# Kernel optimization log

Hardware: AMD Instinct MI355X
Metric: run time of the kernel (lower is better)

## Reference

```python
import jax, jax.numpy as jnp
import numpy as np

DIM = 128

def setup_inputs() -> dict:
    key = jax.random.key(0)
    ks = jax.random.split(key, 4)
    N, C, L = 64, DIM, 4096
    scale = 1.0 / np.sqrt(DIM)
    return {
        "x": jax.random.normal(ks[0], (N, C, L), dtype=jnp.float32),
        "Wq": jax.random.normal(ks[1], (DIM, DIM), dtype=jnp.float32) * scale,
        "bq": jnp.zeros((DIM,), dtype=jnp.float32),
        "Wk": jax.random.normal(ks[2], (DIM, DIM), dtype=jnp.float32) * scale,
        "bk": jnp.zeros((DIM,), dtype=jnp.float32),
        "Wv": jax.random.normal(ks[3], (DIM, DIM), dtype=jnp.float32) * scale,
        "bv": jnp.zeros((DIM,), dtype=jnp.float32),
    }

def reference(x, Wq, bq, Wk, bk, Wv, bv):
    # x: [N, C, L] -> rearrange to [N, L, C]
    h = jnp.transpose(x, (0, 2, 1))                       # [N, L, C]
    q = jnp.einsum('nlc,cd->nld', h, Wq) + bq             # [N, L, D]
    k = jnp.einsum('nlc,cd->nld', h, Wk) + bk             # [N, L, D]
    v = jnp.einsum('nlc,cd->nld', h, Wv) + bv             # [N, L, D]
    # AFT-Simple: softmax over sequence axis of K, global weighted pool of V
    w = jax.nn.softmax(k, axis=1)                         # [N, L, D]
    pooled = jnp.sum(w * v, axis=1, keepdims=True)        # [N, 1, D]
    out = jax.nn.sigmoid(q) * pooled                      # [N, L, D]
    return jnp.transpose(out, (0, 2, 1))                  # [N, C, L]
```

## Files before the change

### kernel.cpp

```cpp
#include <hip/hip_runtime.h>
#include <hip/hip_bf16.h>

#define NB 64
#define CD 128
#define LL 4096
#define LCHUNK 64
#define NCHUNK 64

typedef __attribute__((ext_vector_type(8))) short short8;
typedef __attribute__((ext_vector_type(4))) float f32x4;

#define LOG2E 1.4426950408889634f

#define WT_OFF   0
#define WSS_OFF  (1u<<20)
#define WSP_OFF  ((1u<<20) + NB*NCHUNK*CD*4)
#define POOL_OFF ((1u<<20) + 2u*NB*NCHUNK*CD*4)
#define WSQ_OFF  (8u<<20)

__device__ __forceinline__ unsigned short f2bf(float f) {
    union { float f; unsigned u; } v; v.f = f;
    unsigned r = v.u + 0x7FFFu + ((v.u >> 16) & 1u);
    return (unsigned short)(r >> 16);
}
__device__ __forceinline__ float bf2f(unsigned short h) {
    union { unsigned u; float f; } v; v.u = ((unsigned)h) << 16;
    return v.f;
}
__device__ __forceinline__ unsigned pack2(float lo, float hi) {
    union { __hip_bfloat162 h; unsigned u; } v;
    v.h = __float22bfloat162_rn(float2{lo, hi});
    return v.u;
}

__global__ void prep_wt(const float* __restrict__ Wq, const float* __restrict__ Wk,
                        const float* __restrict__ Wv, unsigned short* __restrict__ wt) {
    int t = blockIdx.x >> 7;
    int d = blockIdx.x & 127;
    const float* W = (t == 0) ? Wq : (t == 1) ? Wk : Wv;
    int c = threadIdx.x;
    wt[((size_t)t*CD + d)*CD + c] = f2bf(W[c*CD + d]);
}

__global__ __launch_bounds__(256, 4)
void aft_pass1(const float* __restrict__ x, const unsigned short* __restrict__ wt,
               const float* __restrict__ bq, const float* __restrict__ bk,
               const float* __restrict__ bv,
               float* __restrict__ wsS, float* __restrict__ wsP,
               unsigned short* __restrict__ wsq) {
    __shared__ char lds_x[64 * 272];
    __shared__ unsigned short lds_q[CD * 68];
    const int tid = threadIdx.x;
    const int n = blockIdx.x >> 6;
    const int ch = blockIdx.x & 63;
    const int l0 = ch * LCHUNK;
    const int w = tid >> 6, lane = tid & 63, r = lane & 15, g = lane >> 4;

    {
        const int f = tid & 15;
        const int tg = tid >> 4;
        const int sw = 16 * 272 * 0 + 0; (void)sw;
#pragma unroll
        for (int it = 0; it < 4; ++it) {
            int cp = tg + 16*it;
            int c0 = 2*cp;
            f32x4 lo = *(const f32x4*)(x + ((size_t)n*CD + c0    )*LL + l0 + 4*f);
            f32x4 hi = *(const f32x4*)(x + ((size_t)n*CD + c0 + 1)*LL + l0 + 4*f);
            int B  = cp >> 2;
            int go = cp & 3;
            char* base = lds_x + (4*f)*272 + 16*(B ^ (f & 7)) + 4*go;
#pragma unroll
            for (int j = 0; j < 4; ++j)
                *(unsigned*)(base + j*272) = pack2(lo[j], hi[j]);
        }
    }

    short8 a_k[2][4], a_v[2][4];
#pragma unroll
    for (int rt = 0; rt < 2; ++rt)
#pragma unroll
        for (int s = 0; s < 4; ++s) {
            int d = 32*w + 16*rt + r;
            a_k[rt][s] = *(const short8*)(wt + ((size_t)(1*CD + d))*CD + 32*s + 8*g);
            a_v[rt][s] = *(const short8*)(wt + ((size_t)(2*CD + d))*CD + 32*s + 8*g);
        }
    f32x4 bkv[2], bvv[2];
#pragma unroll
    for (int rt = 0; rt < 2; ++rt) {
        bkv[rt] = *(const f32x4*)(bk + 32*w + 16*rt + 4*g);
        bvv[rt] = *(const f32x4*)(bv + 32*w + 16*rt + 4*g);
    }

    __syncthreads();

    float s_run[2][4], p_run[2][4];
#pragma unroll
    for (int rt = 0; rt < 2; ++rt)
#pragma unroll
        for (int v = 0; v < 4; ++v) { s_run[rt][v] = 0.f; p_run[rt][v] = 0.f; }

#pragma unroll 1
    for (int ct = 0; ct < 4; ++ct) {
        f32x4 ak[2], av[2];
#pragma unroll
        for (int rt = 0; rt < 2; ++rt) {
            ak[rt] = (f32x4){0.f,0.f,0.f,0.f};
            av[rt] = (f32x4){0.f,0.f,0.f,0.f};
        }
        const int lrow = 16*ct + r;
        const int lsw = (lrow >> 2) & 7;
#pragma unroll
        for (int s = 0; s < 4; ++s) {
            const short8 b = *(const short8*)(lds_x + lrow*272 + 16*((4*s + g) ^ lsw));
            ak[0] = __builtin_amdgcn_mfma_f32_16x16x32_bf16(a_k[0][s], b, ak[0], 0,0,0);
            ak[1] = __builtin_amdgcn_mfma_f32_16x16x32_bf16(a_k[1][s], b, ak[1], 0,0,0);
            av[0] = __builtin_amdgcn_mfma_f32_16x16x32_bf16(a_v[0][s], b, av[0], 0,0,0);
            av[1] = __builtin_amdgcn_mfma_f32_16x16x32_bf16(a_v[1][s], b, av[1], 0,0,0);
        }
#pragma unroll
        for (int rt = 0; rt < 2; ++rt)
#pragma unroll
            for (int v = 0; v < 4; ++v) {
                float e = __builtin_amdgcn_exp2f((ak[rt][v] + bkv[rt][v]) * LOG2E);
                s_run[rt][v] += e;
                p_run[rt][v] += e * (av[rt][v] + bvv[rt][v]);
            }
    }

    short8 a_q[2][4];
#pragma unroll
    for (int rt = 0; rt < 2; ++rt)
#pragma unroll
        for (int s = 0; s < 4; ++s) {
            int d = 32*w + 16*rt + r;
            a_q[rt][s] = *(const short8*)(wt + ((size_t)(0*CD + d))*CD + 32*s + 8*g);
        }
    f32x4 bqv[2];
#pragma unroll
    for (int rt = 0; rt < 2; ++rt)
        bqv[rt] = *(const f32x4*)(bq + 32*w + 16*rt + 4*g);

#pragma unroll 1
    for (int ct = 0; ct < 4; ++ct) {
        f32x4 aq[2];
        aq[0] = (f32x4){0.f,0.f,0.f,0.f};
        aq[1] = (f32x4){0.f,0.f,0.f,0.f};
        const int lrow = 16*ct + r;
        const int lsw = (lrow >> 2) & 7;
#pragma unroll
        for (int s = 0; s < 4; ++s) {
            const short8 b = *(const short8*)(lds_x + lrow*272 + 16*((4*s + g) ^ lsw));
            aq[0] = __builtin_amdgcn_mfma_f32_16x16x32_bf16(a_q[0][s], b, aq[0], 0,0,0);
            aq[1] = __builtin_amdgcn_mfma_f32_16x16x32_bf16(a_q[1][s], b, aq[1], 0,0,0);
        }
#pragma unroll
        for (int rt = 0; rt < 2; ++rt)
#pragma unroll
            for (int v = 0; v < 4; ++v) {
                float q2 = (aq[rt][v] + bqv[rt][v]) * LOG2E;
                float sg = __builtin_amdgcn_rcpf(1.f + __builtin_amdgcn_exp2f(-q2));
                lds_q[(32*w + 16*rt + 4*g + v)*68 + ct*16 + r] = f2bf(sg);
            }
    }

#pragma unroll
    for (int rt = 0; rt < 2; ++rt)
#pragma unroll
        for (int v = 0; v < 4; ++v) {
            float s = s_run[rt][v], p = p_run[rt][v];
#pragma unroll
            for (int mask = 1; mask <= 8; mask <<= 1) {
                s += __shfl_xor(s, mask, 64);
                p += __shfl_xor(p, mask, 64);
            }
            if (r == 0) {
                int d = 32*w + 16*rt + 4*g + v;
                size_t idx = ((size_t)n*NCHUNK + ch)*CD + d;
                wsS[idx] = s;
                wsP[idx] = p;
            }
        }

    __syncthreads();
    {
        unsigned short* tile = wsq + ((size_t)(n*NCHUNK + ch)) * (CD*LCHUNK);
        const int col = tid & 7;
#pragma unroll
        for (int it = 0; it < 4; ++it) {
            int row = (tid >> 3) + 32*it;
            short8 val = *(const short8*)(lds_q + row*68 + 8*col);
            *(short8*)(tile + row*LCHUNK + 8*col) = val;
        }
    }
}

__global__ void aft_pass2(const float* __restrict__ wsS, const float* __restrict__ wsP,
                          float* __restrict__ pooled) {
    int n = blockIdx.x, d = threadIdx.x;
    float s = 0.f, p = 0.f;
    for (int b = 0; b < NCHUNK; ++b) {
        size_t idx = ((size_t)n*NCHUNK + b)*CD + d;
        s += wsS[idx];
        p += wsP[idx];
    }
    pooled[(size_t)n*CD + d] = p / s;
}

__global__ __launch_bounds__(256)
void aft_pass3(const unsigned short* __restrict__ wsq, const float* __restrict__ pooled,
               float* __restrict__ out) {
    __shared__ float lpool[CD];
    const int n = blockIdx.x >> 6;
    const int ch = blockIdx.x & 63;
    if (threadIdx.x < CD) lpool[threadIdx.x] = pooled[(size_t)n*CD + threadIdx.x];
    __syncthreads();
    const unsigned short* tile = wsq + ((size_t)(n*NCHUNK + ch)) * (CD*LCHUNK);
    const int l0 = ch * LCHUNK;
#pragma unroll
    for (int it = 0; it < 4; ++it) {
        int gi = threadIdx.x + 256*it;
        int row = gi >> 3, col = gi & 7;
        short8 v = *(const short8*)(tile + row*LCHUNK + 8*col);
        float pl = lpool[row];
        f32x4 o0, o1;
#pragma unroll
        for (int j = 0; j < 4; ++j) {
            o0[j] = bf2f((unsigned short)v[j]) * pl;
            o1[j] = bf2f((unsigned short)v[4+j]) * pl;
        }
        float* dst = out + ((size_t)n*CD + row)*LL + l0 + 8*col;
        *(f32x4*)dst = o0;
        *(f32x4*)(dst + 4) = o1;
    }
}

extern "C" void kernel_launch(void* const* d_in, const int* in_sizes, int n_in,
                              void* d_out, int out_size, void* d_ws, size_t ws_size,
                              hipStream_t stream) {
    const float* x  = (const float*)d_in[0];
    const float* Wq = (const float*)d_in[1];
    const float* bq = (const float*)d_in[2];
    const float* Wk = (const float*)d_in[3];
    const float* bk = (const float*)d_in[4];
    const float* Wv = (const float*)d_in[5];
    const float* bv = (const float*)d_in[6];
    float* out = (float*)d_out;
    char* ws = (char*)d_ws;
    unsigned short* wt = (unsigned short*)(ws + WT_OFF);
    float* wsS = (float*)(ws + WSS_OFF);
    float* wsP = (float*)(ws + WSP_OFF);
    float* pooled = (float*)(ws + POOL_OFF);
    unsigned short* wsq = (unsigned short*)(ws + WSQ_OFF);

    prep_wt<<<384, 128, 0, stream>>>(Wq, Wk, Wv, wt);
    aft_pass1<<<NB * NCHUNK, 256, 0, stream>>>(x, wt, bq, bk, bv, wsS, wsP, wsq);
    aft_pass2<<<NB, CD, 0, stream>>>(wsS, wsP, pooled);
    aft_pass3<<<NB * NCHUNK, 256, 0, stream>>>(wsq, pooled, out);
}
```

Baseline: 122.1 us.

## Make pass1 persistent over eight chunks with register-prefetched x tiles

Pass1 now launches 512 blocks of 512 threads, and each block loops over 8 consecutive L-chunks. The next chunk's x is prefetched into registers while the current one is computed, and the Q/K/V weight fragments are loaded once per block instead of once per chunk. Q, K and V MFMAs are fused into one loop, the sigmoid tile is packed to bf16 pairs through LDS, and partial sums are reduced per block group, which shrinks the pass2 reduction. The trade-off is fewer blocks (512 vs 4096) and extra barriers per iteration, so occupancy and latency hiding may suffer.

```diff
diff --git a/kernel.cpp b/kernel.cpp
--- a/kernel.cpp
+++ b/kernel.cpp
@@ -6,16 +6,19 @@
 #define LL 4096
 #define LCHUNK 64
 #define NCHUNK 64
+#define NT 8
+#define NBG 8
 
 typedef __attribute__((ext_vector_type(8))) short short8;
 typedef __attribute__((ext_vector_type(4))) float f32x4;
+typedef __attribute__((ext_vector_type(4))) unsigned u32x4;
 
 #define LOG2E 1.4426950408889634f
 
 #define WT_OFF   0
 #define WSS_OFF  (1u<<20)
-#define WSP_OFF  ((1u<<20) + NB*NCHUNK*CD*4)
-#define POOL_OFF ((1u<<20) + 2u*NB*NCHUNK*CD*4)
+#define WSP_OFF  ((1u<<20) + NB*NBG*CD*4)
+#define POOL_OFF ((1u<<20) + 2u*NB*NBG*CD*4)
 #define WSQ_OFF  (8u<<20)
 
 __device__ __forceinline__ unsigned short f2bf(float f) {
@@ -42,154 +45,122 @@
     wt[((size_t)t*CD + d)*CD + c] = f2bf(W[c*CD + d]);
 }
 
-__global__ __launch_bounds__(256, 4)
+__global__ __launch_bounds__(512, 4)
 void aft_pass1(const float* __restrict__ x, const unsigned short* __restrict__ wt,
                const float* __restrict__ bq, const float* __restrict__ bk,
                const float* __restrict__ bv,
                float* __restrict__ wsS, float* __restrict__ wsP,
                unsigned short* __restrict__ wsq) {
     __shared__ char lds_x[64 * 272];
-    __shared__ unsigned short lds_q[CD * 68];
+    __shared__ unsigned lds_t[CD * 33];
     const int tid = threadIdx.x;
-    const int n = blockIdx.x >> 6;
-    const int ch = blockIdx.x & 63;
-    const int l0 = ch * LCHUNK;
-    const int w = tid >> 6, lane = tid & 63, r = lane & 15, g = lane >> 4;
+    const int n = blockIdx.x >> 3;
+    const int bg = blockIdx.x & 7;
+    const int ww = tid >> 6, lane = tid & 63, r = lane & 15, g = lane >> 4;
+    const int f = tid & 15, tg = tid >> 4;
+
+    short8 a_q[4], a_k[4], a_v[4];
+#pragma unroll
+    for (int s = 0; s < 4; ++s) {
+        int d = 16*ww + r;
+        a_q[s] = *(const short8*)(wt + ((size_t)(0*CD + d))*CD + 32*s + 8*g);
+        a_k[s] = *(const short8*)(wt + ((size_t)(1*CD + d))*CD + 32*s + 8*g);
+        a_v[s] = *(const short8*)(wt + ((size_t)(2*CD + d))*CD + 32*s + 8*g);
+    }
+    const f32x4 bqv = *(const f32x4*)(bq + 16*ww + 4*g);
+    const f32x4 bkv = *(const f32x4*)(bk + 16*ww + 4*g);
+    const f32x4 bvv = *(const f32x4*)(bv + 16*ww + 4*g);
+
+    float s_run[4] = {0.f,0.f,0.f,0.f}, p_run[4] = {0.f,0.f,0.f,0.f};
+
+    f32x4 rx0, rx1, rx2, rx3;
+    const size_t xbase = (size_t)n*CD*LL;
 
     {
-        const int f = tid & 15;
-        const int tg = tid >> 4;
-        const int sw = 16 * 272 * 0 + 0; (void)sw;
-#pragma unroll
-        for (int it = 0; it < 4; ++it) {
-            int cp = tg + 16*it;
-            int c0 = 2*cp;
-            f32x4 lo = *(const f32x4*)(x + ((size_t)n*CD + c0    )*LL + l0 + 4*f);
-            f32x4 hi = *(const f32x4*)(x + ((size_t)n*CD + c0 + 1)*LL + l0 + 4*f);
-            int B  = cp >> 2;
-            int go = cp & 3;
-            char* base = lds_x + (4*f)*272 + 16*(B ^ (f & 7)) + 4*go;
-#pragma unroll
-            for (int j = 0; j < 4; ++j)
-                *(unsigned*)(base + j*272) = pack2(lo[j], hi[j]);
-        }
-    }
-
-    short8 a_k[2][4], a_v[2][4];
-#pragma unroll
-    for (int rt = 0; rt < 2; ++rt)
-#pragma unroll
-        for (int s = 0; s < 4; ++s) {
-            int d = 32*w + 16*rt + r;
-            a_k[rt][s] = *(const short8*)(wt + ((size_t)(1*CD + d))*CD + 32*s + 8*g);
-            a_v[rt][s] = *(const short8*)(wt + ((size_t)(2*CD + d))*CD + 32*s + 8*g);
-        }
-    f32x4 bkv[2], bvv[2];
-#pragma unroll
-    for (int rt = 0; rt < 2; ++rt) {
-        bkv[rt] = *(const f32x4*)(bk + 32*w + 16*rt + 4*g);
-        bvv[rt] = *(const f32x4*)(bv + 32*w + 16*rt + 4*g);
-    }
-
-    __syncthreads();
-
-    float s_run[2][4], p_run[2][4];
-#pragma unroll
-    for (int rt = 0; rt < 2; ++rt)
-#pragma unroll
-        for (int v = 0; v < 4; ++v) { s_run[rt][v] = 0.f; p_run[rt][v] = 0.f; }
-
-#pragma unroll 1
-    for (int ct = 0; ct < 4; ++ct) {
-        f32x4 ak[2], av[2];
-#pragma unroll
-        for (int rt = 0; rt < 2; ++rt) {
-            ak[rt] = (f32x4){0.f,0.f,0.f,0.f};
-            av[rt] = (f32x4){0.f,0.f,0.f,0.f};
-        }
-        const int lrow = 16*ct + r;
-        const int lsw = (lrow >> 2) & 7;
-#pragma unroll
-        for (int s = 0; s < 4; ++s) {
-            const short8 b = *(const short8*)(lds_x + lrow*272 + 16*((4*s + g) ^ lsw));
-            ak[0] = __builtin_amdgcn_mfma_f32_16x16x32_bf16(a_k[0][s], b, ak[0], 0,0,0);
-            ak[1] = __builtin_amdgcn_mfma_f32_16x16x32_bf16(a_k[1][s], b, ak[1], 0,0,0);
-            av[0] = __builtin_amdgcn_mfma_f32_16x16x32_bf16(a_v[0][s], b, av[0], 0,0,0);
-            av[1] = __builtin_amdgcn_mfma_f32_16x16x32_bf16(a_v[1][s], b, av[1], 0,0,0);
-        }
-#pragma unroll
-        for (int rt = 0; rt < 2; ++rt)
+        const int l0 = (bg*NT) * LCHUNK;
+        rx0 = *(const f32x4*)(x + xbase + (size_t)(2*tg    )*LL + l0 + 4*f);
+        rx1 = *(const f32x4*)(x + xbase + (size_t)(2*tg + 1)*LL + l0 + 4*f);
+        rx2 = *(const f32x4*)(x + xbase + (size_t)(2*(tg+32)    )*LL + l0 + 4*f);
+        rx3 = *(const f32x4*)(x + xbase + (size_t)(2*(tg+32) + 1)*LL + l0 + 4*f);
+    }
+
+    for (int t = 0; t < NT; ++t) {
+        const int ch = bg*NT + t;
+        __syncthreads();
+        {
+            char* base0 = lds_x + (4*f)*272 + 16*((tg>>2) ^ (f & 7)) + 4*(tg & 3);
+            char* base1 = lds_x + (4*f)*272 + 16*(((tg+32)>>2) ^ (f & 7)) + 4*((tg+32) & 3);
+#pragma unroll
+            for (int j = 0; j < 4; ++j) {
+                *(unsigned*)(base0 + j*272) = pack2(rx0[j], rx1[j]);
+                *(unsigned*)(base1 + j*272) = pack2(rx2[j], rx3[j]);
+            }
+        }
+        __syncthreads();
+        if (t + 1 < NT) {
+            const int l0 = (ch + 1) * LCHUNK;
+            rx0 = *(const f32x4*)(x + xbase + (size_t)(2*tg    )*LL + l0 + 4*f);
+            rx1 = *(const f32x4*)(x + xbase + (size_t)(2*tg + 1)*LL + l0 + 4*f);
+            rx2 = *(const f32x4*)(x + xbase + (size_t)(2*(tg+32)    )*LL + l0 + 4*f);
+            rx3 = *(const f32x4*)(x + xbase + (size_t)(2*(tg+32) + 1)*LL + l0 + 4*f);
+        }
+#pragma unroll
+        for (int ct = 0; ct < 4; ++ct) {
+            f32x4 aq = (f32x4){0.f,0.f,0.f,0.f};
+            f32x4 ak = (f32x4){0.f,0.f,0.f,0.f};
+            f32x4 av = (f32x4){0.f,0.f,0.f,0.f};
+            const int lrow = 16*ct + r;
+            const int lsw = (lrow >> 2) & 7;
+#pragma unroll
+            for (int s = 0; s < 4; ++s) {
+                const short8 b = *(const short8*)(lds_x + lrow*272 + 16*((4*s + g) ^ lsw));
+                aq = __builtin_amdgcn_mfma_f32_16x16x32_bf16(a_q[s], b, aq, 0,0,0);
+                ak = __builtin_amdgcn_mfma_f32_16x16x32_bf16(a_k[s], b, ak, 0,0,0);
+                av = __builtin_amdgcn_mfma_f32_16x16x32_bf16(a_v[s], b, av, 0,0,0);
+            }
+            float sg[4];
 #pragma unroll
             for (int v = 0; v < 4; ++v) {
-                float e = __builtin_amdgcn_exp2f((ak[rt][v] + bkv[rt][v]) * LOG2E);
-                s_run[rt][v] += e;
-                p_run[rt][v] += e * (av[rt][v] + bvv[rt][v]);
-            }
-    }
-
-    short8 a_q[2][4];
-#pragma unroll
-    for (int rt = 0; rt < 2; ++rt)
-#pragma unroll
-        for (int s = 0; s < 4; ++s) {
-            int d = 32*w + 16*rt + r;
-            a_q[rt][s] = *(const short8*)(wt + ((size_t)(0*CD + d))*CD + 32*s + 8*g);
-        }
-    f32x4 bqv[2];
-#pragma unroll
-    for (int rt = 0; rt < 2; ++rt)
-        bqv[rt] = *(const f32x4*)(bq + 32*w + 16*rt + 4*g);
-
-#pragma unroll 1
-    for (int ct = 0; ct < 4; ++ct) {
-        f32x4 aq[2];
-        aq[0] = (f32x4){0.f,0.f,0.f,0.f};
-        aq[1] = (f32x4){0.f,0.f,0.f,0.f};
-        const int lrow = 16*ct + r;
-        const int lsw = (lrow >> 2) & 7;
-#pragma unroll
-        for (int s = 0; s < 4; ++s) {
-            const short8 b = *(const short8*)(lds_x + lrow*272 + 16*((4*s + g) ^ lsw));
-            aq[0] = __builtin_amdgcn_mfma_f32_16x16x32_bf16(a_q[0][s], b, aq[0], 0,0,0);
-            aq[1] = __builtin_amdgcn_mfma_f32_16x16x32_bf16(a_q[1][s], b, aq[1], 0,0,0);
-        }
-#pragma unroll
-        for (int rt = 0; rt < 2; ++rt)
+                float e = __builtin_amdgcn_exp2f((ak[v] + bkv[v]) * LOG2E);
+                s_run[v] += e;
+                p_run[v] += e * (av[v] + bvv[v]);
+                float q2 = (aq[v] + bqv[v]) * LOG2E;
+                sg[v] = __builtin_amdgcn_rcpf(1.f + __builtin_amdgcn_exp2f(-q2));
+            }
 #pragma unroll
             for (int v = 0; v < 4; ++v) {
-                float q2 = (aq[rt][v] + bqv[rt][v]) * LOG2E;
-                float sg = __builtin_amdgcn_rcpf(1.f + __builtin_amdgcn_exp2f(-q2));
-                lds_q[(32*w + 16*rt + 4*g + v)*68 + ct*16 + r] = f2bf(sg);
-            }
-    }
-
-#pragma unroll
-    for (int rt = 0; rt < 2; ++rt)
-#pragma unroll
-        for (int v = 0; v < 4; ++v) {
-            float s = s_run[rt][v], p = p_run[rt][v];
-#pragma unroll
-            for (int mask = 1; mask <= 8; mask <<= 1) {
-                s += __shfl_xor(s, mask, 64);
-                p += __shfl_xor(p, mask, 64);
-            }
-            if (r == 0) {
-                int d = 32*w + 16*rt + 4*g + v;
-                size_t idx = ((size_t)n*NCHUNK + ch)*CD + d;
-                wsS[idx] = s;
-                wsP[idx] = p;
-            }
-        }
-
-    __syncthreads();
-    {
-        unsigned short* tile = wsq + ((size_t)(n*NCHUNK + ch)) * (CD*LCHUNK);
-        const int col = tid & 7;
-#pragma unroll
-        for (int it = 0; it < 4; ++it) {
-            int row = (tid >> 3) + 32*it;
-            short8 val = *(const short8*)(lds_q + row*68 + 8*col);
-            *(short8*)(tile + row*LCHUNK + 8*col) = val;
+                float other = __shfl_xor(sg[v], 1, 64);
+                if (!(lane & 1))
+                    lds_t[(16*ww + 4*g + v)*33 + 8*ct + (r >> 1)] = pack2(sg[v], other);
+            }
+        }
+        __syncthreads();
+        {
+            unsigned short* tile = wsq + ((size_t)(n*NCHUNK + ch)) * (CD*LCHUNK);
+            const int row = tid >> 2, part = tid & 3;
+            const unsigned* src = lds_t + row*33 + part*8;
+            u32x4 A, B;
+#pragma unroll
+            for (int k = 0; k < 4; ++k) { A[k] = src[k]; B[k] = src[4+k]; }
+            unsigned short* dst = tile + row*LCHUNK + part*16;
+            *(u32x4*)dst = A;
+            *(u32x4*)(dst + 8) = B;
+        }
+    }
+
+#pragma unroll
+    for (int v = 0; v < 4; ++v) {
+        float s = s_run[v], p = p_run[v];
+#pragma unroll
+        for (int mask = 1; mask <= 8; mask <<= 1) {
+            s += __shfl_xor(s, mask, 64);
+            p += __shfl_xor(p, mask, 64);
+        }
+        if (r == 0) {
+            int d = 16*ww + 4*g + v;
+            size_t idx = ((size_t)n*NBG + bg)*CD + d;
+            wsS[idx] = s;
+            wsP[idx] = p;
         }
     }
 }
@@ -198,8 +169,8 @@
                           float* __restrict__ pooled) {
     int n = blockIdx.x, d = threadIdx.x;
     float s = 0.f, p = 0.f;
-    for (int b = 0; b < NCHUNK; ++b) {
-        size_t idx = ((size_t)n*NCHUNK + b)*CD + d;
+    for (int b = 0; b < NBG; ++b) {
+        size_t idx = ((size_t)n*NBG + b)*CD + d;
         s += wsS[idx];
         p += wsP[idx];
     }
@@ -253,7 +224,7 @@
     unsigned short* wsq = (unsigned short*)(ws + WSQ_OFF);
 
     prep_wt<<<384, 128, 0, stream>>>(Wq, Wk, Wv, wt);
-    aft_pass1<<<NB * NCHUNK, 256, 0, stream>>>(x, wt, bq, bk, bv, wsS, wsP, wsq);
+    aft_pass1<<<NB * NBG, 512, 0, stream>>>(x, wt, bq, bk, bv, wsS, wsP, wsq);
     aft_pass2<<<NB, CD, 0, stream>>>(wsS, wsP, pooled);
     aft_pass3<<<NB * NCHUNK, 256, 0, stream>>>(wsq, pooled, out);
 }
```

New measurement: 162.0 us. 1.33x slower.

## Recompute q from x in output pass instead of storing bf16 q workspace

Applied to the files above, without the earlier changes.

Splits the first pass into a K/V-only reduction kernel and moves the Q projection plus sigmoid into the final output kernel, which re-stages x and writes the output directly. This removes the bf16 q write and read through global workspace but re-reads x a second time. MFMA operands are swapped so each lane owns a feature column, simplifying the cross-lane reduction and bias loads.

```diff
diff --git a/kernel.cpp b/kernel.cpp
--- a/kernel.cpp
+++ b/kernel.cpp
@@ -16,16 +16,11 @@
 #define WSS_OFF  (1u<<20)
 #define WSP_OFF  ((1u<<20) + NB*NCHUNK*CD*4)
 #define POOL_OFF ((1u<<20) + 2u*NB*NCHUNK*CD*4)
-#define WSQ_OFF  (8u<<20)
 
 __device__ __forceinline__ unsigned short f2bf(float f) {
     union { float f; unsigned u; } v; v.f = f;
     unsigned r = v.u + 0x7FFFu + ((v.u >> 16) & 1u);
     return (unsigned short)(r >> 16);
-}
-__device__ __forceinline__ float bf2f(unsigned short h) {
-    union { unsigned u; float f; } v; v.u = ((unsigned)h) << 16;
-    return v.f;
 }
 __device__ __forceinline__ unsigned pack2(float lo, float hi) {
     union { __hip_bfloat162 h; unsigned u; } v;
@@ -42,154 +37,88 @@
     wt[((size_t)t*CD + d)*CD + c] = f2bf(W[c*CD + d]);
 }
 
+__device__ __forceinline__ void stage_x(const float* __restrict__ x, char* lds_x,
+                                        int n, int l0, int tid) {
+    const int f = tid & 15, tg = tid >> 4;
+#pragma unroll
+    for (int it = 0; it < 4; ++it) {
+        int cp = tg + 16*it;
+        f32x4 lo = *(const f32x4*)(x + ((size_t)n*CD + 2*cp    )*LL + l0 + 4*f);
+        f32x4 hi = *(const f32x4*)(x + ((size_t)n*CD + 2*cp + 1)*LL + l0 + 4*f);
+        char* base = lds_x + (4*f)*272 + 16*((cp >> 2) ^ (f & 7)) + 4*(cp & 3);
+#pragma unroll
+        for (int j = 0; j < 4; ++j)
+            *(unsigned*)(base + j*272) = pack2(lo[j], hi[j]);
+    }
+}
+
 __global__ __launch_bounds__(256, 4)
-void aft_pass1(const float* __restrict__ x, const unsigned short* __restrict__ wt,
-               const float* __restrict__ bq, const float* __restrict__ bk,
-               const float* __restrict__ bv,
-               float* __restrict__ wsS, float* __restrict__ wsP,
-               unsigned short* __restrict__ wsq) {
+void aft_kv(const float* __restrict__ x, const unsigned short* __restrict__ wt,
+            const float* __restrict__ bk, const float* __restrict__ bv,
+            float* __restrict__ wsS, float* __restrict__ wsP) {
     __shared__ char lds_x[64 * 272];
-    __shared__ unsigned short lds_q[CD * 68];
     const int tid = threadIdx.x;
     const int n = blockIdx.x >> 6;
     const int ch = blockIdx.x & 63;
     const int l0 = ch * LCHUNK;
     const int w = tid >> 6, lane = tid & 63, r = lane & 15, g = lane >> 4;
 
-    {
-        const int f = tid & 15;
-        const int tg = tid >> 4;
-        const int sw = 16 * 272 * 0 + 0; (void)sw;
-#pragma unroll
-        for (int it = 0; it < 4; ++it) {
-            int cp = tg + 16*it;
-            int c0 = 2*cp;
-            f32x4 lo = *(const f32x4*)(x + ((size_t)n*CD + c0    )*LL + l0 + 4*f);
-            f32x4 hi = *(const f32x4*)(x + ((size_t)n*CD + c0 + 1)*LL + l0 + 4*f);
-            int B  = cp >> 2;
-            int go = cp & 3;
-            char* base = lds_x + (4*f)*272 + 16*(B ^ (f & 7)) + 4*go;
-#pragma unroll
-            for (int j = 0; j < 4; ++j)
-                *(unsigned*)(base + j*272) = pack2(lo[j], hi[j]);
-        }
-    }
-
-    short8 a_k[2][4], a_v[2][4];
-#pragma unroll
-    for (int rt = 0; rt < 2; ++rt)
+    short8 b_k[2][4], b_v[2][4];
+    float bkl[2], bvl[2];
+#pragma unroll
+    for (int dt = 0; dt < 2; ++dt) {
+        int d = 32*w + 16*dt + r;
 #pragma unroll
         for (int s = 0; s < 4; ++s) {
-            int d = 32*w + 16*rt + r;
-            a_k[rt][s] = *(const short8*)(wt + ((size_t)(1*CD + d))*CD + 32*s + 8*g);
-            a_v[rt][s] = *(const short8*)(wt + ((size_t)(2*CD + d))*CD + 32*s + 8*g);
-        }
-    f32x4 bkv[2], bvv[2];
-#pragma unroll
-    for (int rt = 0; rt < 2; ++rt) {
-        bkv[rt] = *(const f32x4*)(bk + 32*w + 16*rt + 4*g);
-        bvv[rt] = *(const f32x4*)(bv + 32*w + 16*rt + 4*g);
-    }
-
+            b_k[dt][s] = *(const short8*)(wt + ((size_t)(1*CD + d))*CD + 32*s + 8*g);
+            b_v[dt][s] = *(const short8*)(wt + ((size_t)(2*CD + d))*CD + 32*s + 8*g);
+        }
+        bkl[dt] = bk[d];
+        bvl[dt] = bv[d];
+    }
+
+    stage_x(x, lds_x, n, l0, tid);
     __syncthreads();
 
-    float s_run[2][4], p_run[2][4];
-#pragma unroll
-    for (int rt = 0; rt < 2; ++rt)
-#pragma unroll
-        for (int v = 0; v < 4; ++v) { s_run[rt][v] = 0.f; p_run[rt][v] = 0.f; }
-
-#pragma unroll 1
-    for (int ct = 0; ct < 4; ++ct) {
+    float s_run[2] = {0.f, 0.f}, p_run[2] = {0.f, 0.f};
+
+#pragma unroll
+    for (int lt = 0; lt < 4; ++lt) {
+        const int lrow = 16*lt + r;
+        const int lsw = (lrow >> 2) & 7;
+        short8 a[4];
+#pragma unroll
+        for (int s = 0; s < 4; ++s)
+            a[s] = *(const short8*)(lds_x + lrow*272 + 16*((4*s + g) ^ lsw));
         f32x4 ak[2], av[2];
 #pragma unroll
-        for (int rt = 0; rt < 2; ++rt) {
-            ak[rt] = (f32x4){0.f,0.f,0.f,0.f};
-            av[rt] = (f32x4){0.f,0.f,0.f,0.f};
-        }
-        const int lrow = 16*ct + r;
-        const int lsw = (lrow >> 2) & 7;
+        for (int dt = 0; dt < 2; ++dt) { ak[dt] = (f32x4){0,0,0,0}; av[dt] = (f32x4){0,0,0,0}; }
 #pragma unroll
         for (int s = 0; s < 4; ++s) {
-            const short8 b = *(const short8*)(lds_x + lrow*272 + 16*((4*s + g) ^ lsw));
-            ak[0] = __builtin_amdgcn_mfma_f32_16x16x32_bf16(a_k[0][s], b, ak[0], 0,0,0);
-            ak[1] = __builtin_amdgcn_mfma_f32_16x16x32_bf16(a_k[1][s], b, ak[1], 0,0,0);
-            av[0] = __builtin_amdgcn_mfma_f32_16x16x32_bf16(a_v[0][s], b, av[0], 0,0,0);
-            av[1] = __builtin_amdgcn_mfma_f32_16x16x32_bf16(a_v[1][s], b, av[1], 0,0,0);
-        }
-#pragma unroll
-        for (int rt = 0; rt < 2; ++rt)
+            ak[0] = __builtin_amdgcn_mfma_f32_16x16x32_bf16(a[s], b_k[0][s], ak[0], 0,0,0);
+            ak[1] = __builtin_amdgcn_mfma_f32_16x16x32_bf16(a[s], b_k[1][s], ak[1], 0,0,0);
+            av[0] = __builtin_amdgcn_mfma_f32_16x16x32_bf16(a[s], b_v[0][s], av[0], 0,0,0);
+            av[1] = __builtin_amdgcn_mfma_f32_16x16x32_bf16(a[s], b_v[1][s], av[1], 0,0,0);
+        }
+#pragma unroll
+        for (int dt = 0; dt < 2; ++dt)
 #pragma unroll
             for (int v = 0; v < 4; ++v) {
-                float e = __builtin_amdgcn_exp2f((ak[rt][v] + bkv[rt][v]) * LOG2E);
-                s_run[rt][v] += e;
-                p_run[rt][v] += e * (av[rt][v] + bvv[rt][v]);
+                float e = __builtin_amdgcn_exp2f((ak[dt][v] + bkl[dt]) * LOG2E);
+                s_run[dt] += e;
+                p_run[dt] += e * (av[dt][v] + bvl[dt]);
             }
     }
 
-    short8 a_q[2][4];
-#pragma unroll
-    for (int rt = 0; rt < 2; ++rt)
-#pragma unroll
-        for (int s = 0; s < 4; ++s) {
-            int d = 32*w + 16*rt + r;
-            a_q[rt][s] = *(const short8*)(wt + ((size_t)(0*CD + d))*CD + 32*s + 8*g);
-        }
-    f32x4 bqv[2];
-#pragma unroll
-    for (int rt = 0; rt < 2; ++rt)
-        bqv[rt] = *(const f32x4*)(bq + 32*w + 16*rt + 4*g);
-
-#pragma unroll 1
-    for (int ct = 0; ct < 4; ++ct) {
-        f32x4 aq[2];
-        aq[0] = (f32x4){0.f,0.f,0.f,0.f};
-        aq[1] = (f32x4){0.f,0.f,0.f,0.f};
-        const int lrow = 16*ct + r;
-        const int lsw = (lrow >> 2) & 7;
-#pragma unroll
-        for (int s = 0; s < 4; ++s) {
-            const short8 b = *(const short8*)(lds_x + lrow*272 + 16*((4*s + g) ^ lsw));
-            aq[0] = __builtin_amdgcn_mfma_f32_16x16x32_bf16(a_q[0][s], b, aq[0], 0,0,0);
-            aq[1] = __builtin_amdgcn_mfma_f32_16x16x32_bf16(a_q[1][s], b, aq[1], 0,0,0);
-        }
-#pragma unroll
-        for (int rt = 0; rt < 2; ++rt)
-#pragma unroll
-            for (int v = 0; v < 4; ++v) {
-                float q2 = (aq[rt][v] + bqv[rt][v]) * LOG2E;
-                float sg = __builtin_amdgcn_rcpf(1.f + __builtin_amdgcn_exp2f(-q2));
-                lds_q[(32*w + 16*rt + 4*g + v)*68 + ct*16 + r] = f2bf(sg);
-            }
-    }
-
-#pragma unroll
-    for (int rt = 0; rt < 2; ++rt)
-#pragma unroll
-        for (int v = 0; v < 4; ++v) {
-            float s = s_run[rt][v], p = p_run[rt][v];
-#pragma unroll
-            for (int mask = 1; mask <= 8; mask <<= 1) {
-                s += __shfl_xor(s, mask, 64);
-                p += __shfl_xor(p, mask, 64);
-            }
-            if (r == 0) {
-                int d = 32*w + 16*rt + 4*g + v;
-                size_t idx = ((size_t)n*NCHUNK + ch)*CD + d;
-                wsS[idx] = s;
-                wsP[idx] = p;
-            }
-        }
-
-    __syncthreads();
-    {
-        unsigned short* tile = wsq + ((size_t)(n*NCHUNK + ch)) * (CD*LCHUNK);
-        const int col = tid & 7;
-#pragma unroll
-        for (int it = 0; it < 4; ++it) {
-            int row = (tid >> 3) + 32*it;
-            short8 val = *(const short8*)(lds_q + row*68 + 8*col);
-            *(short8*)(tile + row*LCHUNK + 8*col) = val;
+#pragma unroll
+    for (int dt = 0; dt < 2; ++dt) {
+        float s = s_run[dt], p = p_run[dt];
+        s += __shfl_xor(s, 16, 64);  p += __shfl_xor(p, 16, 64);
+        s += __shfl_xor(s, 32, 64);  p += __shfl_xor(p, 32, 64);
+        if (g == 0) {
+            size_t idx = ((size_t)n*NCHUNK + ch)*CD + 32*w + 16*dt + r;
+            wsS[idx] = s;
+            wsP[idx] = p;
         }
     }
 }
@@ -206,31 +135,58 @@
     pooled[(size_t)n*CD + d] = p / s;
 }
 
-__global__ __launch_bounds__(256)
-void aft_pass3(const unsigned short* __restrict__ wsq, const float* __restrict__ pooled,
-               float* __restrict__ out) {
-    __shared__ float lpool[CD];
+__global__ __launch_bounds__(256, 4)
+void aft_q(const float* __restrict__ x, const unsigned short* __restrict__ wt,
+           const float* __restrict__ bq, const float* __restrict__ pooled,
+           float* __restrict__ out) {
+    __shared__ char lds_x[64 * 272];
+    const int tid = threadIdx.x;
     const int n = blockIdx.x >> 6;
     const int ch = blockIdx.x & 63;
-    if (threadIdx.x < CD) lpool[threadIdx.x] = pooled[(size_t)n*CD + threadIdx.x];
+    const int l0 = ch * LCHUNK;
+    const int w = tid >> 6, lane = tid & 63, r = lane & 15, g = lane >> 4;
+
+    short8 b_q[2][4];
+    float bql[2], pll[2];
+#pragma unroll
+    for (int dt = 0; dt < 2; ++dt) {
+        int d = 32*w + 16*dt + r;
+#pragma unroll
+        for (int s = 0; s < 4; ++s)
+            b_q[dt][s] = *(const short8*)(wt + ((size_t)(0*CD + d))*CD + 32*s + 8*g);
+        bql[dt] = bq[d];
+        pll[dt] = pooled[(size_t)n*CD + d];
+    }
+
+    stage_x(x, lds_x, n, l0, tid);
     __syncthreads();
-    const unsigned short* tile = wsq + ((size_t)(n*NCHUNK + ch)) * (CD*LCHUNK);
-    const int l0 = ch * LCHUNK;
-#pragma unroll
-    for (int it = 0; it < 4; ++it) {
-        int gi = threadIdx.x + 256*it;
-        int row = gi >> 3, col = gi & 7;
-        short8 v = *(const short8*)(tile + row*LCHUNK + 8*col);
-        float pl = lpool[row];
-        f32x4 o0, o1;
-#pragma unroll
-        for (int j = 0; j < 4; ++j) {
-            o0[j] = bf2f((unsigned short)v[j]) * pl;
-            o1[j] = bf2f((unsigned short)v[4+j]) * pl;
-        }
-        float* dst = out + ((size_t)n*CD + row)*LL + l0 + 8*col;
-        *(f32x4*)dst = o0;
-        *(f32x4*)(dst + 4) = o1;
+
+#pragma unroll
+    for (int lt = 0; lt < 4; ++lt) {
+        const int lrow = 16*lt + r;
+        const int lsw = (lrow >> 2) & 7;
+        short8 a[4];
+#pragma unroll
+        for (int s = 0; s < 4; ++s)
+            a[s] = *(const short8*)(lds_x + lrow*272 + 16*((4*s + g) ^ lsw));
+        f32x4 aq[2];
+        aq[0] = (f32x4){0,0,0,0};
+        aq[1] = (f32x4){0,0,0,0};
+#pragma unroll
+        for (int s = 0; s < 4; ++s) {
+            aq[0] = __builtin_amdgcn_mfma_f32_16x16x32_bf16(a[s], b_q[0][s], aq[0], 0,0,0);
+            aq[1] = __builtin_amdgcn_mfma_f32_16x16x32_bf16(a[s], b_q[1][s], aq[1], 0,0,0);
+        }
+#pragma unroll
+        for (int dt = 0; dt < 2; ++dt) {
+            f32x4 o;
+#pragma unroll
+            for (int v = 0; v < 4; ++v) {
+                float q2 = (aq[dt][v] + bql[dt]) * LOG2E;
+                o[v] = pll[dt] * __builtin_amdgcn_rcpf(1.f + __builtin_amdgcn_exp2f(-q2));
+            }
+            *(f32x4*)(out + ((size_t)n*CD + 32*w + 16*dt + r)*LL + l0 + 16*lt + 4*g) = o;
+        }
     }
 }
 
@@ -250,10 +206,9 @@
     float* wsS = (float*)(ws + WSS_OFF);
     float* wsP = (float*)(ws + WSP_OFF);
     float* pooled = (float*)(ws + POOL_OFF);
-    unsigned short* wsq = (unsigned short*)(ws + WSQ_OFF);
 
     prep_wt<<<384, 128, 0, stream>>>(Wq, Wk, Wv, wt);
-    aft_pass1<<<NB * NCHUNK, 256, 0, stream>>>(x, wt, bq, bk, bv, wsS, wsP, wsq);
+    aft_kv<<<NB * NCHUNK, 256, 0, stream>>>(x, wt, bk, bv, wsS, wsP);
     aft_pass2<<<NB, CD, 0, stream>>>(wsS, wsP, pooled);
-    aft_pass3<<<NB * NCHUNK, 256, 0, stream>>>(wsq, pooled, out);
-}
+    aft_q<<<NB * NCHUNK, 256, 0, stream>>>(x, wt, bq, pooled, out);
+}
```

New measurement: 101.6 us. 1.2x faster.
